# Kernel tuning notes

Measured on AMD Instinct MI355X. Metric: run time of the kernel, lower is better.

## Reference

```python
import jax, jax.numpy as jnp
import numpy as np

NUM_NODES = 4
WEIGHT = 2
IN_C = 128
OUT_C = 128
N = 128
T = 512
BN_EPS = 1e-5


def _shift_index(A, node_num, channels, weight):
    """Faithful numpy port of Modified_shift_gcn.shift(). A: binarized [V,V]."""
    idx = np.arange(node_num * channels).reshape(node_num, channels)
    idx_copy = idx.copy()
    for i in range(node_num):
        current_A = A[i].copy()
        current_A[i] = 0
        neighbors = np.nonzero(current_A)[0]
        j = 0
        counter_i = i + 1
        while j < channels:
            next_node = counter_i % node_num
            if j < weight:
                j += weight
            elif next_node == i:
                j += weight
                counter_i += 1
            elif next_node in neighbors:
                idx[i][j:j + weight] = idx_copy[next_node][j:j + weight]
                j += weight
                counter_i += 1
            else:
                idx[i][j] = idx_copy[next_node][j]
                j += 1
                counter_i += 1
    return idx.flatten()


def setup_inputs() -> dict:
    key = jax.random.key(0)
    k1, k2 = jax.random.split(key)
    # A summed over num_subset then binarized, as in __init__
    adj = np.array([[0, 1, 0, 1], [1, 0, 1, 0], [0, 1, 0, 1], [1, 0, 1, 0]], dtype=np.float64)
    A = np.stack([adj, adj, adj]).sum(0)
    A = (A != 0).astype(np.float64)
    shift_in = jnp.asarray(_shift_index(A.copy(), NUM_NODES, IN_C, WEIGHT), dtype=jnp.int32)
    shift_out = jnp.asarray(_shift_index(A.copy(), NUM_NODES, OUT_C, WEIGHT), dtype=jnp.int32)
    x = jax.random.normal(k1, (N, IN_C, T, NUM_NODES), dtype=jnp.float32)
    Linear_weight = jax.random.normal(k2, (IN_C, OUT_C), dtype=jnp.float32) * float(np.sqrt(1.0 / OUT_C))
    Linear_bias = jnp.zeros((1, 1, OUT_C), dtype=jnp.float32)
    Feature_Mask = jnp.zeros((1, NUM_NODES, IN_C), dtype=jnp.float32)
    bn_gamma = jnp.ones((NUM_NODES * OUT_C,), dtype=jnp.float32)
    bn_beta = jnp.zeros((NUM_NODES * OUT_C,), dtype=jnp.float32)
    return {"x": x, "Linear_weight": Linear_weight, "Linear_bias": Linear_bias,
            "Feature_Mask": Feature_Mask, "bn_gamma": bn_gamma, "bn_beta": bn_beta,
            "shift_in": shift_in, "shift_out": shift_out}


def reference(x, Linear_weight, Linear_bias, Feature_Mask, bn_gamma, bn_beta, shift_in, shift_out):
    n, c, t, v = x.shape
    d = Linear_weight.shape[1]
    # [N,C,T,V] -> [N*T, V*C]
    h = jnp.transpose(x, (0, 2, 3, 1)).reshape(n * t, v * c)
    # shift-in gather
    h = jnp.take(h, shift_in, axis=1)
    # feature mask (tanh + 1) and pointwise linear over channels
    h = h.reshape(n * t, v, c) * (jnp.tanh(Feature_Mask) + 1.0)
    h = jnp.einsum('nvc,cd->nvd', h, Linear_weight) + Linear_bias
    # shift-out gather
    h = h.reshape(n * t, v * d)
    h = jnp.take(h, shift_out, axis=1)
    # BatchNorm1d over the N*T batch dim (training-mode batch stats, biased var)
    mean = jnp.mean(h, axis=0)
    var = jnp.mean(jnp.square(h - mean), axis=0)
    h = (h - mean) * jax.lax.rsqrt(var + BN_EPS) * bn_gamma + bn_beta
    # back to [N,C_out,T,V], residual (down is identity since in==out), ReLU
    out = jnp.transpose(h.reshape(n, t, v, d), (0, 3, 1, 2))
    return jax.nn.relu(out + x)
```

## Files before the change

### kernel.cpp

```cpp
#include <hip/hip_runtime.h>

typedef __attribute__((ext_vector_type(4))) float f32x4;
typedef __attribute__((ext_vector_type(8))) short s16x8;

#define DEV __device__ __forceinline__

namespace {
constexpr int CH = 128;
constexpr int TDIM = 512;
constexpr int NBLK = 512;
constexpr float INV_ROWS = 1.0f / 65536.0f;
constexpr float EPS = 1e-5f;

DEV unsigned short f2bf(float f) {
  unsigned int u = __float_as_uint(f);
  u = (u + 0x7FFFu + ((u >> 16) & 1u)) >> 16;
  return (unsigned short)u;
}
DEV float bf2f(unsigned short s) { return __uint_as_float(((unsigned int)s) << 16); }

DEV float maskval(float x) { return 2.0f / (1.0f + __expf(-2.0f * x)); }

DEV int xgi(int b, int v, int t, int c) {
  return (((b << 2) + v) * 16 + t) * 128 + (c ^ ((t & 7) << 3));
}
}

template <int PHASE>
__global__ __launch_bounds__(512) void gcn_fused(
    const float* __restrict__ x, const float* __restrict__ W,
    const float* __restrict__ FM, const int* __restrict__ shin,
    const int* __restrict__ shout, const float* __restrict__ tab,
    float* __restrict__ part, float* __restrict__ out) {
  __shared__ __align__(16) unsigned short xg[2 * 4 * 16 * 128];

  const int tid = threadIdx.x;
  const int lane = tid & 63;
  const int w = tid >> 6;
  const int g4 = lane >> 4;
  const int l16 = lane & 15;
  const int dbase = w * 16;

  const int bid = blockIdx.x;
  const int n = bid >> 2;
  const int tb = (bid & 3) * 128;

  const int tlow = tid & 7;
  const int cp = tid >> 3;
  const int c0 = cp * 2;

  float mk[2][4];
  unsigned int svp = 0;
#pragma unroll
  for (int i = 0; i < 2; ++i)
#pragma unroll
    for (int v = 0; v < 4; ++v) {
      int j = v * CH + (c0 + i);
      mk[i][v] = maskval(FM[j]);
      svp |= (unsigned int)((shin[j] >> 7) & 3) << ((i * 4 + v) * 2);
    }

  s16x8 wt[4];
#pragma unroll
  for (int kk = 0; kk < 4; ++kk) {
    s16x8 f;
#pragma unroll
    for (int e = 0; e < 8; ++e)
      f[e] = (short)f2bf(W[(kk * 32 + g4 * 8 + e) * CH + dbase + l16]);
    wt[kk] = f;
  }

  unsigned int svo = 0;
  if (PHASE == 2) {
#pragma unroll
    for (int r = 0; r < 4; ++r) {
      int d = dbase + g4 * 4 + r;
#pragma unroll
      for (int v = 0; v < 4; ++v)
        svo |= (unsigned int)((shout[v * CH + d] >> 7) & 3) << (r * 8 + v * 2);
    }
  }

  float s2[4][4];
  f32x4 rs[2];
  if (PHASE == 1) {
#pragma unroll
    for (int vo = 0; vo < 4; ++vo)
#pragma unroll
      for (int r = 0; r < 4; ++r) s2[vo][r] = 0.f;
    rs[0] = f32x4{0.f, 0.f, 0.f, 0.f};
    rs[1] = f32x4{0.f, 0.f, 0.f, 0.f};
  }

  const f32x4* xf4 = (const f32x4*)x;
  const float2* tab2 = (const float2*)tab;

  f32x4 pa[2][2], pb[2][2];

#define LOADT(SLOT, TILE)                                                       \
  {                                                                             \
    _Pragma("unroll") for (int h = 0; h < 2; ++h) {                             \
      const int tgl = tb + (TILE) * 16 + h * 8 + tlow;                          \
      pa[SLOT][h] = xf4[(n * CH + c0) * TDIM + tgl];                            \
      pb[SLOT][h] = xf4[(n * CH + c0 + 1) * TDIM + tgl];                        \
    }                                                                           \
  }

#define STAGE(BUF, SLOT)                                                        \
  {                                                                             \
    _Pragma("unroll") for (int h = 0; h < 2; ++h) {                             \
      const int t = h * 8 + tlow;                                               \
      if (PHASE == 1) {                                                         \
        rs[0] += pa[SLOT][h];                                                   \
        rs[1] += pb[SLOT][h];                                                   \
      }                                                                         \
      _Pragma("unroll") for (int v = 0; v < 4; ++v) {                           \
        int s0 = (svp >> ((0 * 4 + v) * 2)) & 3;                                \
        float a = pa[SLOT][h][0];                                               \
        a = (s0 == 1) ? pa[SLOT][h][1] : a;                                     \
        a = (s0 == 2) ? pa[SLOT][h][2] : a;                                     \
        a = (s0 == 3) ? pa[SLOT][h][3] : a;                                     \
        a *= mk[0][v];                                                          \
        int s1 = (svp >> ((1 * 4 + v) * 2)) & 3;                                \
        float b = pb[SLOT][h][0];                                               \
        b = (s1 == 1) ? pb[SLOT][h][1] : b;                                     \
        b = (s1 == 2) ? pb[SLOT][h][2] : b;                                     \
        b = (s1 == 3) ? pb[SLOT][h][3] : b;                                     \
        b *= mk[1][v];                                                          \
        *(unsigned int*)&xg[xgi(BUF, v, t, c0)] =                               \
            (unsigned int)f2bf(a) | ((unsigned int)f2bf(b) << 16);              \
      }                                                                         \
    }                                                                           \
  }

  {
    LOADT(0, 0)
    LOADT(1, 1)
    STAGE(0, 0)
  }

#pragma unroll
  for (int tile = 0; tile < 8; ++tile) {
    const int buf = tile & 1;
    __syncthreads();

    const int tg = tb + tile * 16 + l16;
    f32x4 res[4];
    if (PHASE == 2) {
#pragma unroll
      for (int r = 0; r < 4; ++r) res[r] = xf4[(n * CH + dbase + g4 * 4 + r) * TDIM + tg];
    }
    if (tile < 6) LOADT(buf, tile + 2)

    f32x4 acc[4];
    const f32x4 z4 = {0.f, 0.f, 0.f, 0.f};
#pragma unroll
    for (int vo = 0; vo < 4; ++vo) acc[vo] = z4;
#pragma unroll
    for (int vo = 0; vo < 4; ++vo) {
      s16x8 bfr[4];
#pragma unroll
      for (int kk = 0; kk < 4; ++kk)
        bfr[kk] = *(const s16x8*)&xg[xgi(buf, vo, l16, kk * 32 + g4 * 8)];
#pragma unroll
      for (int kk = 0; kk < 4; ++kk)
        acc[vo] = __builtin_amdgcn_mfma_f32_16x16x32_bf16(wt[kk], bfr[kk], acc[vo], 0, 0, 0);
    }

    if (PHASE == 1) {
#pragma unroll
      for (int vo = 0; vo < 4; ++vo)
#pragma unroll
        for (int r = 0; r < 4; ++r) s2[vo][r] = fmaf(acc[vo][r], acc[vo][r], s2[vo][r]);
    } else {
#pragma unroll
      for (int r = 0; r < 4; ++r) {
        const int d = dbase + g4 * 4 + r;
        f32x4 o;
#pragma unroll
        for (int v = 0; v < 4; ++v) {
          int sv = (svo >> (r * 8 + v * 2)) & 3;
          float ov = acc[0][r];
          ov = (sv == 1) ? acc[1][r] : ov;
          ov = (sv == 2) ? acc[2][r] : ov;
          ov = (sv == 3) ? acc[3][r] : ov;
          float2 ssv = tab2[v * CH + d];
          float y = fmaf(ov, ssv.x, ssv.y) + res[r][v];
          o[v] = fmaxf(y, 0.f);
        }
        *(f32x4*)&out[((n * CH + d) * TDIM + tg) * 4] = o;
      }
    }

    if (tile < 7) STAGE(buf ^ 1, buf ^ 1)
  }
#undef STAGE
#undef LOADT

  if (PHASE == 1) {
#pragma unroll
    for (int vo = 0; vo < 4; ++vo)
#pragma unroll
      for (int r = 0; r < 4; ++r) {
        float v = s2[vo][r];
        v += __shfl_xor(v, 1, 64);
        v += __shfl_xor(v, 2, 64);
        v += __shfl_xor(v, 4, 64);
        v += __shfl_xor(v, 8, 64);
        if (l16 == 0) part[(vo * CH + dbase + g4 * 4 + r) * NBLK + bid] = v;
      }
#pragma unroll
    for (int i = 0; i < 2; ++i)
#pragma unroll
      for (int v = 0; v < 4; ++v) {
        float vv = rs[i][v];
        vv += __shfl_xor(vv, 1, 64);
        vv += __shfl_xor(vv, 2, 64);
        vv += __shfl_xor(vv, 4, 64);
        if (tlow == 0) part[(512 + (c0 + i) * 4 + v) * NBLK + bid] = vv;
      }
  }
}

__global__ __launch_bounds__(256) void gcn_reduce(const float* __restrict__ part,
                                                  float* __restrict__ sums) {
  __shared__ float acc4[4];
  const int r = blockIdx.x;
  const int t = threadIdx.x;
  const float* row = part + r * NBLK;
  float s = row[t] + row[t + 256];
#pragma unroll
  for (int off = 1; off < 64; off <<= 1) s += __shfl_xor(s, off, 64);
  if ((t & 63) == 0) acc4[t >> 6] = s;
  __syncthreads();
  if (t == 0) sums[r] = acc4[0] + acc4[1] + acc4[2] + acc4[3];
}

__global__ void gcn_finalize(const float* __restrict__ sums,
                             const float* __restrict__ W,
                             const float* __restrict__ FM,
                             const int* __restrict__ shin,
                             const int* __restrict__ shout,
                             const float* __restrict__ gamma,
                             const float* __restrict__ beta,
                             float* __restrict__ tab) {
  __shared__ float q[512];
  __shared__ float meanS[512];
  __shared__ float rstdS[512];
  const int j = threadIdx.x;
  const int vo = j >> 7;
  const int c = j & 127;
  const int sv = (shin[j] >> 7) & 3;
  q[j] = maskval(FM[j]) * sums[512 + c * 4 + sv];
  __syncthreads();
  const int d = c;
  float acc = 0.f;
#pragma unroll 8
  for (int cc = 0; cc < 128; ++cc) acc = fmaf(W[cc * CH + d], q[vo * CH + cc], acc);
  const float mean = acc * INV_ROWS;
  const float var = sums[j] * INV_ROWS - mean * mean;
  meanS[j] = mean;
  rstdS[j] = rsqrtf(var + EPS);
  __syncthreads();
  const int so = shout[j];
  const float sc = rstdS[so] * gamma[j];
  const float sh = beta[j] - meanS[so] * sc;
  tab[2 * j] = sc;
  tab[2 * j + 1] = sh;
}

extern "C" void kernel_launch(void* const* d_in, const int* in_sizes, int n_in,
                              void* d_out, int out_size, void* d_ws, size_t ws_size,
                              hipStream_t stream) {
  const float* x = (const float*)d_in[0];
  const float* W = (const float*)d_in[1];
  const float* FM = (const float*)d_in[3];
  const float* gamma = (const float*)d_in[4];
  const float* beta = (const float*)d_in[5];
  const int* shin = (const int*)d_in[6];
  const int* shout = (const int*)d_in[7];
  float* out = (float*)d_out;

  float* part = (float*)d_ws;
  float* sums = part + 1024 * NBLK;
  float* tab = sums + 1024;

  gcn_fused<1><<<dim3(NBLK), dim3(512), 0, stream>>>(x, W, FM, shin, shout, tab, part, out);
  gcn_reduce<<<dim3(1024), dim3(256), 0, stream>>>(part, sums);
  gcn_finalize<<<dim3(1), dim3(512), 0, stream>>>(sums, W, FM, shin, shout, gamma, beta, tab);
  gcn_fused<2><<<dim3(NBLK), dim3(512), 0, stream>>>(x, W, FM, shin, shout, tab, part, out);
}
```

Measured before the change: 108.8 us.

## Merge stats, reduce, finalize and output passes into one cooperative kernel

Replaces the four-kernel sequence with a single cooperative launch of 256 blocks, each handling two work units, using grid syncs between the statistics pass, the partial-sum reduction and the output pass. Every block recomputes the BN scale/shift table redundantly into shared memory instead of a separate single-block finalize kernel. This removes launch gaps and the tiny serial finalize kernel. It also adds a cheaper paired bf16 pack via a perm instruction, which truncates with a fixed rounding bias instead of round-to-nearest-even. The costs are grid-sync overhead, only 256 blocks occupying the GPU, and redundant finalize work in every block.

```diff
diff --git a/kernel.cpp b/kernel.cpp
--- a/kernel.cpp
+++ b/kernel.cpp
@@ -1,4 +1,7 @@
 #include <hip/hip_runtime.h>
+#include <hip/hip_cooperative_groups.h>
+
+namespace cg = cooperative_groups;
 
 typedef __attribute__((ext_vector_type(4))) float f32x4;
 typedef __attribute__((ext_vector_type(8))) short s16x8;
@@ -8,7 +11,7 @@
 namespace {
 constexpr int CH = 128;
 constexpr int TDIM = 512;
-constexpr int NBLK = 512;
+constexpr int NBLK = 256;
 constexpr float INV_ROWS = 1.0f / 65536.0f;
 constexpr float EPS = 1e-5f;
 
@@ -17,7 +20,16 @@
   u = (u + 0x7FFFu + ((u >> 16) & 1u)) >> 16;
   return (unsigned short)u;
 }
-DEV float bf2f(unsigned short s) { return __uint_as_float(((unsigned int)s) << 16); }
+
+DEV unsigned int pack2bf(float lo, float hi) {
+  unsigned int ua = __float_as_uint(lo) + 0x8000u;
+  unsigned int ub = __float_as_uint(hi) + 0x8000u;
+#if __has_builtin(__builtin_amdgcn_perm)
+  return __builtin_amdgcn_perm(ub, ua, 0x07060302u);
+#else
+  return (ub & 0xFFFF0000u) | (ua >> 16);
+#endif
+}
 
 DEV float maskval(float x) { return 2.0f / (1.0f + __expf(-2.0f * x)); }
 
@@ -26,13 +38,17 @@
 }
 }
 
-template <int PHASE>
-__global__ __launch_bounds__(512) void gcn_fused(
+__global__ __launch_bounds__(512) void gcn_all(
     const float* __restrict__ x, const float* __restrict__ W,
     const float* __restrict__ FM, const int* __restrict__ shin,
-    const int* __restrict__ shout, const float* __restrict__ tab,
-    float* __restrict__ part, float* __restrict__ out) {
+    const int* __restrict__ shout, const float* __restrict__ gamma,
+    const float* __restrict__ beta, float* __restrict__ part,
+    float* __restrict__ sums, float* __restrict__ out) {
   __shared__ __align__(16) unsigned short xg[2 * 4 * 16 * 128];
+  __shared__ float q[512];
+  __shared__ float meanS[512];
+  __shared__ float rstdS[512];
+  __shared__ float2 tabL[512];
 
   const int tid = threadIdx.x;
   const int lane = tid & 63;
@@ -42,12 +58,10 @@
   const int dbase = w * 16;
 
   const int bid = blockIdx.x;
-  const int n = bid >> 2;
-  const int tb = (bid & 3) * 128;
+  int n = 0, tb = 0;
 
   const int tlow = tid & 7;
-  const int cp = tid >> 3;
-  const int c0 = cp * 2;
+  const int c0 = (tid >> 3) * 2;
 
   float mk[2][4];
   unsigned int svp = 0;
@@ -71,133 +85,101 @@
   }
 
   unsigned int svo = 0;
-  if (PHASE == 2) {
-#pragma unroll
-    for (int r = 0; r < 4; ++r) {
-      int d = dbase + g4 * 4 + r;
-#pragma unroll
-      for (int v = 0; v < 4; ++v)
-        svo |= (unsigned int)((shout[v * CH + d] >> 7) & 3) << (r * 8 + v * 2);
-    }
-  }
-
-  float s2[4][4];
-  f32x4 rs[2];
-  if (PHASE == 1) {
+#pragma unroll
+  for (int r = 0; r < 4; ++r) {
+    int d = dbase + g4 * 4 + r;
+#pragma unroll
+    for (int v = 0; v < 4; ++v)
+      svo |= (unsigned int)((shout[v * CH + d] >> 7) & 3) << (r * 8 + v * 2);
+  }
+
+  const f32x4* xf4 = (const f32x4*)x;
+  f32x4 pa[2][2], pb[2][2];
+
+#define LOADT(SLOT, TILE)                                                 \
+  {                                                                       \
+    _Pragma("unroll") for (int h = 0; h < 2; ++h) {                       \
+      const int tgl = tb + (TILE) * 16 + h * 8 + tlow;                    \
+      pa[SLOT][h] = xf4[(n * CH + c0) * TDIM + tgl];                      \
+      pb[SLOT][h] = xf4[(n * CH + c0 + 1) * TDIM + tgl];                  \
+    }                                                                     \
+  }
+
+#define STAGE(BUF, SLOT, ACCRS)                                           \
+  {                                                                       \
+    _Pragma("unroll") for (int h = 0; h < 2; ++h) {                       \
+      const int t = h * 8 + tlow;                                         \
+      if (ACCRS) {                                                        \
+        rs[0] += pa[SLOT][h];                                             \
+        rs[1] += pb[SLOT][h];                                             \
+      }                                                                   \
+      _Pragma("unroll") for (int v = 0; v < 4; ++v) {                     \
+        int s0 = (svp >> ((0 * 4 + v) * 2)) & 3;                          \
+        float a = pa[SLOT][h][0];                                         \
+        a = (s0 == 1) ? pa[SLOT][h][1] : a;                               \
+        a = (s0 == 2) ? pa[SLOT][h][2] : a;                               \
+        a = (s0 == 3) ? pa[SLOT][h][3] : a;                               \
+        a *= mk[0][v];                                                    \
+        int s1 = (svp >> ((1 * 4 + v) * 2)) & 3;                          \
+        float b = pb[SLOT][h][0];                                         \
+        b = (s1 == 1) ? pb[SLOT][h][1] : b;                               \
+        b = (s1 == 2) ? pb[SLOT][h][2] : b;                               \
+        b = (s1 == 3) ? pb[SLOT][h][3] : b;                               \
+        b *= mk[1][v];                                                    \
+        *(unsigned int*)&xg[xgi(BUF, v, t, c0)] = pack2bf(a, b);          \
+      }                                                                   \
+    }                                                                     \
+  }
+
+#define MFMA_TILE(BUF)                                                    \
+  {                                                                       \
+    _Pragma("unroll") for (int vo = 0; vo < 4; ++vo) {                    \
+      s16x8 bfr[4];                                                       \
+      _Pragma("unroll") for (int kk = 0; kk < 4; ++kk) bfr[kk] =          \
+          *(const s16x8*)&xg[xgi(BUF, vo, l16, kk * 32 + g4 * 8)];        \
+      _Pragma("unroll") for (int kk = 0; kk < 4; ++kk) acc[vo] =          \
+          __builtin_amdgcn_mfma_f32_16x16x32_bf16(wt[kk], bfr[kk],        \
+                                                  acc[vo], 0, 0, 0);      \
+    }                                                                     \
+  }
+
+  {
+    float s2[4][4];
+    f32x4 rs[2];
 #pragma unroll
     for (int vo = 0; vo < 4; ++vo)
 #pragma unroll
       for (int r = 0; r < 4; ++r) s2[vo][r] = 0.f;
     rs[0] = f32x4{0.f, 0.f, 0.f, 0.f};
     rs[1] = f32x4{0.f, 0.f, 0.f, 0.f};
-  }
-
-  const f32x4* xf4 = (const f32x4*)x;
-  const float2* tab2 = (const float2*)tab;
-
-  f32x4 pa[2][2], pb[2][2];
-
-#define LOADT(SLOT, TILE)                                                       \
-  {                                                                             \
-    _Pragma("unroll") for (int h = 0; h < 2; ++h) {                             \
-      const int tgl = tb + (TILE) * 16 + h * 8 + tlow;                          \
-      pa[SLOT][h] = xf4[(n * CH + c0) * TDIM + tgl];                            \
-      pb[SLOT][h] = xf4[(n * CH + c0 + 1) * TDIM + tgl];                        \
-    }                                                                           \
-  }
-
-#define STAGE(BUF, SLOT)                                                        \
-  {                                                                             \
-    _Pragma("unroll") for (int h = 0; h < 2; ++h) {                             \
-      const int t = h * 8 + tlow;                                               \
-      if (PHASE == 1) {                                                         \
-        rs[0] += pa[SLOT][h];                                                   \
-        rs[1] += pb[SLOT][h];                                                   \
-      }                                                                         \
-      _Pragma("unroll") for (int v = 0; v < 4; ++v) {                           \
-        int s0 = (svp >> ((0 * 4 + v) * 2)) & 3;                                \
-        float a = pa[SLOT][h][0];                                               \
-        a = (s0 == 1) ? pa[SLOT][h][1] : a;                                     \
-        a = (s0 == 2) ? pa[SLOT][h][2] : a;                                     \
-        a = (s0 == 3) ? pa[SLOT][h][3] : a;                                     \
-        a *= mk[0][v];                                                          \
-        int s1 = (svp >> ((1 * 4 + v) * 2)) & 3;                                \
-        float b = pb[SLOT][h][0];                                               \
-        b = (s1 == 1) ? pb[SLOT][h][1] : b;                                     \
-        b = (s1 == 2) ? pb[SLOT][h][2] : b;                                     \
-        b = (s1 == 3) ? pb[SLOT][h][3] : b;                                     \
-        b *= mk[1][v];                                                          \
-        *(unsigned int*)&xg[xgi(BUF, v, t, c0)] =                               \
-            (unsigned int)f2bf(a) | ((unsigned int)f2bf(b) << 16);              \
-      }                                                                         \
-    }                                                                           \
-  }
-
-  {
-    LOADT(0, 0)
-    LOADT(1, 1)
-    STAGE(0, 0)
-  }
-
-#pragma unroll
-  for (int tile = 0; tile < 8; ++tile) {
-    const int buf = tile & 1;
-    __syncthreads();
-
-    const int tg = tb + tile * 16 + l16;
-    f32x4 res[4];
-    if (PHASE == 2) {
-#pragma unroll
-      for (int r = 0; r < 4; ++r) res[r] = xf4[(n * CH + dbase + g4 * 4 + r) * TDIM + tg];
-    }
-    if (tile < 6) LOADT(buf, tile + 2)
-
-    f32x4 acc[4];
-    const f32x4 z4 = {0.f, 0.f, 0.f, 0.f};
-#pragma unroll
-    for (int vo = 0; vo < 4; ++vo) acc[vo] = z4;
-#pragma unroll
-    for (int vo = 0; vo < 4; ++vo) {
-      s16x8 bfr[4];
-#pragma unroll
-      for (int kk = 0; kk < 4; ++kk)
-        bfr[kk] = *(const s16x8*)&xg[xgi(buf, vo, l16, kk * 32 + g4 * 8)];
-#pragma unroll
-      for (int kk = 0; kk < 4; ++kk)
-        acc[vo] = __builtin_amdgcn_mfma_f32_16x16x32_bf16(wt[kk], bfr[kk], acc[vo], 0, 0, 0);
-    }
-
-    if (PHASE == 1) {
-#pragma unroll
-      for (int vo = 0; vo < 4; ++vo)
-#pragma unroll
-        for (int r = 0; r < 4; ++r) s2[vo][r] = fmaf(acc[vo][r], acc[vo][r], s2[vo][r]);
-    } else {
-#pragma unroll
-      for (int r = 0; r < 4; ++r) {
-        const int d = dbase + g4 * 4 + r;
-        f32x4 o;
-#pragma unroll
-        for (int v = 0; v < 4; ++v) {
-          int sv = (svo >> (r * 8 + v * 2)) & 3;
-          float ov = acc[0][r];
-          ov = (sv == 1) ? acc[1][r] : ov;
-          ov = (sv == 2) ? acc[2][r] : ov;
-          ov = (sv == 3) ? acc[3][r] : ov;
-          float2 ssv = tab2[v * CH + d];
-          float y = fmaf(ov, ssv.x, ssv.y) + res[r][v];
-          o[v] = fmaxf(y, 0.f);
-        }
-        *(f32x4*)&out[((n * CH + d) * TDIM + tg) * 4] = o;
+
+    for (int u = 0; u < 2; ++u) {
+      const int unit = bid + u * NBLK;
+      n = unit >> 2;
+      tb = (unit & 3) * 128;
+
+      LOADT(0, 0)
+      LOADT(1, 1)
+      STAGE(0, 0, 1)
+
+#pragma unroll
+      for (int tile = 0; tile < 8; ++tile) {
+        const int buf = tile & 1;
+        __syncthreads();
+        if (tile < 6) LOADT(buf, tile + 2)
+        f32x4 acc[4];
+        const f32x4 z4 = {0.f, 0.f, 0.f, 0.f};
+#pragma unroll
+        for (int vo = 0; vo < 4; ++vo) acc[vo] = z4;
+        MFMA_TILE(buf)
+#pragma unroll
+        for (int vo = 0; vo < 4; ++vo)
+#pragma unroll
+          for (int r = 0; r < 4; ++r) s2[vo][r] = fmaf(acc[vo][r], acc[vo][r], s2[vo][r]);
+        if (tile < 7) STAGE(buf ^ 1, buf ^ 1, 1)
       }
     }
 
-    if (tile < 7) STAGE(buf ^ 1, buf ^ 1)
-  }
-#undef STAGE
-#undef LOADT
-
-  if (PHASE == 1) {
 #pragma unroll
     for (int vo = 0; vo < 4; ++vo)
 #pragma unroll
@@ -220,53 +202,108 @@
         if (tlow == 0) part[(512 + (c0 + i) * 4 + v) * NBLK + bid] = vv;
       }
   }
-}
-
-__global__ __launch_bounds__(256) void gcn_reduce(const float* __restrict__ part,
-                                                  float* __restrict__ sums) {
-  __shared__ float acc4[4];
-  const int r = blockIdx.x;
-  const int t = threadIdx.x;
-  const float* row = part + r * NBLK;
-  float s = row[t] + row[t + 256];
-#pragma unroll
-  for (int off = 1; off < 64; off <<= 1) s += __shfl_xor(s, off, 64);
-  if ((t & 63) == 0) acc4[t >> 6] = s;
+
+  __threadfence();
+  cg::this_grid().sync();
+
+#pragma unroll
+  for (int rr = 0; rr < 4; ++rr) {
+    const int row = bid * 4 + rr;
+    float s = (tid < NBLK) ? part[row * NBLK + tid] : 0.f;
+#pragma unroll
+    for (int off = 1; off < 64; off <<= 1) s += __shfl_xor(s, off, 64);
+    if (lane == 0) q[w] = s;
+    __syncthreads();
+    if (tid == 0) {
+      float t8 = 0.f;
+#pragma unroll
+      for (int i = 0; i < 8; ++i) t8 += q[i];
+      sums[row] = t8;
+    }
+    __syncthreads();
+  }
+
+  __threadfence();
+  cg::this_grid().sync();
+
+  {
+    const int j = tid;
+    const int c = j & 127;
+    const int sv = (shin[j] >> 7) & 3;
+    q[j] = maskval(FM[j]) * sums[512 + c * 4 + sv];
+  }
   __syncthreads();
-  if (t == 0) sums[r] = acc4[0] + acc4[1] + acc4[2] + acc4[3];
-}
-
-__global__ void gcn_finalize(const float* __restrict__ sums,
-                             const float* __restrict__ W,
-                             const float* __restrict__ FM,
-                             const int* __restrict__ shin,
-                             const int* __restrict__ shout,
-                             const float* __restrict__ gamma,
-                             const float* __restrict__ beta,
-                             float* __restrict__ tab) {
-  __shared__ float q[512];
-  __shared__ float meanS[512];
-  __shared__ float rstdS[512];
-  const int j = threadIdx.x;
-  const int vo = j >> 7;
-  const int c = j & 127;
-  const int sv = (shin[j] >> 7) & 3;
-  q[j] = maskval(FM[j]) * sums[512 + c * 4 + sv];
+  {
+    const int j = tid;
+    const int vo = j >> 7;
+    const int d = j & 127;
+    float acc = 0.f;
+#pragma unroll 8
+    for (int cc = 0; cc < 128; ++cc) acc = fmaf(W[cc * CH + d], q[vo * CH + cc], acc);
+    const float mean = acc * INV_ROWS;
+    const float var = sums[j] * INV_ROWS - mean * mean;
+    meanS[j] = mean;
+    rstdS[j] = rsqrtf(var + EPS);
+  }
   __syncthreads();
-  const int d = c;
-  float acc = 0.f;
-#pragma unroll 8
-  for (int cc = 0; cc < 128; ++cc) acc = fmaf(W[cc * CH + d], q[vo * CH + cc], acc);
-  const float mean = acc * INV_ROWS;
-  const float var = sums[j] * INV_ROWS - mean * mean;
-  meanS[j] = mean;
-  rstdS[j] = rsqrtf(var + EPS);
+  {
+    const int j = tid;
+    const int so = shout[j];
+    const float sc = rstdS[so] * gamma[j];
+    const float sh = beta[j] - meanS[so] * sc;
+    tabL[j] = float2{sc, sh};
+  }
   __syncthreads();
-  const int so = shout[j];
-  const float sc = rstdS[so] * gamma[j];
-  const float sh = beta[j] - meanS[so] * sc;
-  tab[2 * j] = sc;
-  tab[2 * j + 1] = sh;
+
+  {
+    f32x4 rs[2];
+    for (int u = 0; u < 2; ++u) {
+      const int unit = bid + u * NBLK;
+      n = unit >> 2;
+      tb = (unit & 3) * 128;
+
+      LOADT(0, 0)
+      LOADT(1, 1)
+      STAGE(0, 0, 0)
+
+#pragma unroll
+      for (int tile = 0; tile < 8; ++tile) {
+        const int buf = tile & 1;
+        __syncthreads();
+        const int tg = tb + tile * 16 + l16;
+        f32x4 res[4];
+#pragma unroll
+        for (int r = 0; r < 4; ++r) res[r] = xf4[(n * CH + dbase + g4 * 4 + r) * TDIM + tg];
+        if (tile < 6) LOADT(buf, tile + 2)
+        f32x4 acc[4];
+        const f32x4 z4 = {0.f, 0.f, 0.f, 0.f};
+#pragma unroll
+        for (int vo = 0; vo < 4; ++vo) acc[vo] = z4;
+        MFMA_TILE(buf)
+#pragma unroll
+        for (int r = 0; r < 4; ++r) {
+          const int d = dbase + g4 * 4 + r;
+          f32x4 o;
+#pragma unroll
+          for (int v = 0; v < 4; ++v) {
+            int sv = (svo >> (r * 8 + v * 2)) & 3;
+            float ov = acc[0][r];
+            ov = (sv == 1) ? acc[1][r] : ov;
+            ov = (sv == 2) ? acc[2][r] : ov;
+            ov = (sv == 3) ? acc[3][r] : ov;
+            float2 ssv = tabL[v * CH + d];
+            float y = fmaf(ov, ssv.x, ssv.y) + res[r][v];
+            o[v] = fmaxf(y, 0.f);
+          }
+          *(f32x4*)&out[((n * CH + d) * TDIM + tg) * 4] = o;
+        }
+        if (tile < 7) STAGE(buf ^ 1, buf ^ 1, 0)
+      }
+    }
+  }
+#undef STAGE
+#undef LOADT
+#undef MFMA_TILE
 }
 
 extern "C" void kernel_launch(void* const* d_in, const int* in_sizes, int n_in,
@@ -283,10 +320,9 @@
 
   float* part = (float*)d_ws;
   float* sums = part + 1024 * NBLK;
-  float* tab = sums + 1024;
-
-  gcn_fused<1><<<dim3(NBLK), dim3(512), 0, stream>>>(x, W, FM, shin, shout, tab, part, out);
-  gcn_reduce<<<dim3(1024), dim3(256), 0, stream>>>(part, sums);
-  gcn_finalize<<<dim3(1), dim3(512), 0, stream>>>(sums, W, FM, shin, shout, gamma, beta, tab);
-  gcn_fused<2><<<dim3(NBLK), dim3(512), 0, stream>>>(x, W, FM, shin, shout, tab, part, out);
-}
+
+  void* args[] = {(void*)&x,     (void*)&W,     (void*)&FM,   (void*)&shin,
+                  (void*)&shout, (void*)&gamma, (void*)&beta, (void*)&part,
+                  (void*)&sums,  (void*)&out};
+  hipLaunchCooperativeKernel((void*)gcn_all, dim3(NBLK), dim3(512), args, 0, stream);
+}
```

Measured after the change: 243.2 us. +123.5%, slower.
